# Kernel optimization log

Hardware: AMD Instinct MI355X
Metric: run time of the kernel (lower is better)

## Reference

```python
import jax, jax.numpy as jnp
import numpy as np

N, C, K, STEPS = 131072, 256, 5, 20


def setup_inputs() -> dict:
    key = jax.random.key(0)
    k1, k2, k3, k4 = jax.random.split(key, 4)
    drive = jax.random.uniform(k1, (N, C), dtype=jnp.float32)  # sigmoid-like drive in [0,1]
    K_raw = jax.random.uniform(k2, (K,), dtype=jnp.float32)
    K_local = K_raw / K_raw.sum()  # positive, sums to 1
    W = jax.random.uniform(k3, (C, C), dtype=jnp.float32)
    mask = (jax.random.uniform(k4, (C, C)) < 0.2).astype(jnp.float32)
    W = W * mask
    W_cc = W / jnp.clip(W.sum(axis=0, keepdims=True), 1e-8)  # column-stochastic
    r = jnp.full((C,), 3.9, dtype=jnp.float32)
    eps = jnp.full((C,), 0.3, dtype=jnp.float32)
    beta = jnp.full((C,), 0.1, dtype=jnp.float32)
    return {"drive": drive, "r": r, "eps": eps, "beta": beta,
            "K_local": K_local, "W_cc": W_cc}


def reference(drive, r, eps, beta, K_local, W_cc):
    # readout == 'final' (module default)
    pad = K // 2
    one_m_eps = 1.0 - eps
    one_m_beta = 1.0 - beta

    def step(grid, _):
        mapped = r * grid * (1.0 - grid)  # [N, C] logistic map
        # circular conv1d over channel axis (cross-correlation, kernel K_local)
        local = K_local[0] * jnp.roll(mapped, pad, axis=-1)
        for j in range(1, K):
            local = local + K_local[j] * jnp.roll(mapped, pad - j, axis=-1)
        global_cc = mapped @ W_cc  # [N, C]
        coupled = 0.5 * (local + global_cc)
        physics = one_m_eps * mapped + eps * coupled
        new_grid = one_m_beta * physics + beta * drive
        return new_grid, None

    grid, _ = jax.lax.scan(step, drive, None, length=STEPS)
    return jnp.clip(grid, 1e-4, 1.0 - 1e-4)
```

## Files before the change

kernel.cpp:

```cpp
#include <hip/hip_runtime.h>

#define C_DIM 256
#define STEPS 20
#define ROWS_PER_WG 32

typedef _Float16 f16;
typedef f16 f16x4 __attribute__((ext_vector_type(4)));
typedef f16 f16x8 __attribute__((ext_vector_type(8)));
typedef float f32x4 __attribute__((ext_vector_type(4)));

__global__ __launch_bounds__(256) void prep_w(const float* __restrict__ W,
                                              const float* __restrict__ Kl,
                                              f16* __restrict__ whi,
                                              f16* __restrict__ wlo)
{
    const int f = (int)(blockIdx.x * blockDim.x + threadIdx.x) >> 6;
    const int l = (int)threadIdx.x & 63;
    if (f >= 128) return;
    const int mt = f >> 3, kb = f & 7;
    const int n = mt * 16 + (l & 15);
    const int kbase = kb * 32 + (l >> 4) * 8;
    f16 h[8], lo[8];
    #pragma unroll
    for (int j = 0; j < 8; ++j) {
        const int k = kbase + j;
        float v = 0.5f * W[k * C_DIM + n];
        const int d = (k - n + 2) & (C_DIM - 1);
        if (d < 5) v += 0.5f * Kl[d];
        const f16 hh = (f16)v;
        h[j] = hh;
        lo[j] = (f16)((v - (float)hh) * 4096.0f);
    }
    const size_t off = (size_t)f * 512 + (size_t)l * 8;
    *(f16x8*)(whi + off) = *(f16x8*)h;
    *(f16x8*)(wlo + off) = *(f16x8*)lo;
}

__global__ __launch_bounds__(512, 2) void cml_main(
    const float* __restrict__ drive,
    const float* __restrict__ r_,
    const float* __restrict__ eps_,
    const float* __restrict__ beta_,
    const f16* __restrict__ whi,
    const f16* __restrict__ wlo,
    float* __restrict__ out)
{
    __shared__ char smem[65536];

    const int tid = (int)threadIdx.x;
    const int w   = tid >> 6;
    const int l   = tid & 63;
    const int kg  = l >> 4;
    const int cl  = l & 15;
    const size_t rowBase = (size_t)blockIdx.x * ROWS_PER_WG;

    f16x8 Wh[2][8], Wl[2][8];
    #pragma unroll
    for (int mti = 0; mti < 2; ++mti) {
        #pragma unroll
        for (int kb = 0; kb < 8; ++kb) {
            const size_t off = (size_t)((w * 2 + mti) * 8 + kb) * 512 + (size_t)l * 8;
            Wh[mti][kb] = *(const f16x8*)(whi + off);
            Wl[mti][kb] = *(const f16x8*)(wlo + off);
        }
    }

    float rr[2][4], P1[2][4], P2[2][4];
    #pragma unroll
    for (int mti = 0; mti < 2; ++mti) {
        const int ch0 = (w * 2 + mti) * 16 + kg * 4;
        #pragma unroll
        for (int r = 0; r < 4; ++r) {
            const int ch = ch0 + r;
            const float rv = r_[ch], ev = eps_[ch], bv = beta_[ch];
            rr[mti][r] = rv;
            P1[mti][r] = (1.0f - bv) * (1.0f - ev);
            P2[mti][r] = (1.0f - bv) * ev;
        }
    }

    float g[2][2][4], m_[2][2][4], drv[2][2][4];
    #pragma unroll
    for (int mti = 0; mti < 2; ++mti) {
        const int ch0 = (w * 2 + mti) * 16 + kg * 4;
        #pragma unroll
        for (int nt = 0; nt < 2; ++nt) {
            const size_t row = rowBase + (size_t)(nt * 16 + cl);
            const f32x4 d4 = *(const f32x4*)(drive + row * C_DIM + ch0);
            #pragma unroll
            for (int r = 0; r < 4; ++r) {
                const float bv = beta_[ch0 + r];
                g[mti][nt][r]   = d4[r];
                drv[mti][nt][r] = bv * d4[r];
            }
        }
    }

    int rbase[2], woff[2][2];
    #pragma unroll
    for (int nt = 0; nt < 2; ++nt) {
        const int m = nt * 16 + cl;
        rbase[nt] = (m << 9) + ((kg ^ (m & 7)) << 4);
        #pragma unroll
        for (int mti = 0; mti < 2; ++mti) {
            const int c = (w * 2 + mti) * 2 + (kg >> 1);
            const int p = c ^ (m & 7);
            woff[mti][nt] = (m << 9) + (p << 4) + ((kg & 1) << 3);
        }
    }

    #pragma unroll
    for (int mti = 0; mti < 2; ++mti) {
        #pragma unroll
        for (int nt = 0; nt < 2; ++nt) {
            f16x4 hv, lv;
            #pragma unroll
            for (int r = 0; r < 4; ++r) {
                const float gv = g[mti][nt][r];
                const float mv = rr[mti][r] * gv * (1.0f - gv);
                m_[mti][nt][r] = mv;
                const f16 hh = (f16)mv;
                hv[r] = hh;
                lv[r] = (f16)((mv - (float)hh) * 4096.0f);
            }
            *(f16x4*)(smem + woff[mti][nt]) = hv;
            *(f16x4*)(smem + woff[mti][nt] + 16384) = lv;
        }
    }

    #pragma unroll 1
    for (int s = 0; s < STEPS; ++s) {
        __syncthreads();
        const int rb = (s & 1) << 15;
        const int wb = rb ^ 32768;

        #pragma unroll
        for (int nt = 0; nt < 2; ++nt) {
            f32x4 acch[2], accl[2];
            #pragma unroll
            for (int mti = 0; mti < 2; ++mti) {
                acch[mti] = (f32x4)0.0f;
                accl[mti] = (f32x4)0.0f;
            }

            const int Ab = rbase[nt] | rb;
            #pragma unroll
            for (int kb = 0; kb < 8; ++kb) {
                const int addr = Ab ^ (kb << 6);
                const f16x8 bh = *(const f16x8*)(smem + addr);
                const f16x8 bl = *(const f16x8*)(smem + addr + 16384);
                #pragma unroll
                for (int mti = 0; mti < 2; ++mti) {
                    acch[mti] = __builtin_amdgcn_mfma_f32_16x16x32_f16(Wh[mti][kb], bh, acch[mti], 0, 0, 0);
                    accl[mti] = __builtin_amdgcn_mfma_f32_16x16x32_f16(Wl[mti][kb], bh, accl[mti], 0, 0, 0);
                    accl[mti] = __builtin_amdgcn_mfma_f32_16x16x32_f16(Wh[mti][kb], bl, accl[mti], 0, 0, 0);
                }
            }

            #pragma unroll
            for (int mti = 0; mti < 2; ++mti) {
                f16x4 hv, lv;
                #pragma unroll
                for (int r = 0; r < 4; ++r) {
                    const float coupled = fmaf(accl[mti][r], 1.0f / 4096.0f, acch[mti][r]);
                    const float gn = fmaf(P1[mti][r], m_[mti][nt][r],
                                     fmaf(P2[mti][r], coupled, drv[mti][nt][r]));
                    g[mti][nt][r] = gn;
                    const float mv = rr[mti][r] * gn * (1.0f - gn);
                    m_[mti][nt][r] = mv;
                    const f16 hh = (f16)mv;
                    hv[r] = hh;
                    lv[r] = (f16)((mv - (float)hh) * 4096.0f);
                }
                if (s != STEPS - 1) {
                    *(f16x4*)(smem + (woff[mti][nt] | wb)) = hv;
                    *(f16x4*)(smem + (woff[mti][nt] | wb) + 16384) = lv;
                }
            }
        }
    }

    #pragma unroll
    for (int mti = 0; mti < 2; ++mti) {
        const int ch0 = (w * 2 + mti) * 16 + kg * 4;
        #pragma unroll
        for (int nt = 0; nt < 2; ++nt) {
            const size_t row = rowBase + (size_t)(nt * 16 + cl);
            f32x4 o;
            #pragma unroll
            for (int r = 0; r < 4; ++r) {
                o[r] = fminf(fmaxf(g[mti][nt][r], 1e-4f), 1.0f - 1e-4f);
            }
            *(f32x4*)(out + row * C_DIM + ch0) = o;
        }
    }
}

extern "C" void kernel_launch(void* const* d_in, const int* in_sizes, int n_in,
                              void* d_out, int out_size, void* d_ws, size_t ws_size,
                              hipStream_t stream) {
    (void)n_in; (void)ws_size; (void)out_size;
    const float* drive = (const float*)d_in[0];
    const float* r     = (const float*)d_in[1];
    const float* eps   = (const float*)d_in[2];
    const float* beta  = (const float*)d_in[3];
    const float* Kl    = (const float*)d_in[4];
    const float* W     = (const float*)d_in[5];
    float* out = (float*)d_out;

    f16* whi = (f16*)d_ws;
    f16* wlo = whi + 65536;

    prep_w<<<dim3(32), dim3(256), 0, stream>>>(W, Kl, whi, wlo);

    const int nrows = in_sizes[0] / C_DIM;
    cml_main<<<dim3((unsigned)(nrows / ROWS_PER_WG)), dim3(512), 0, stream>>>(
        drive, r, eps, beta, whi, wlo, out);
}
```

Baseline: 721.1 us.

## Software-pipeline LDS B loads, stagger row tiles per wave, spill drive term to LDS

The inner MFMA loop now prefetches the next k-block's hi/lo B fragments from LDS while issuing the current MFMAs, and wraps the MFMA group in s_setprio. Half of the waves process the two row tiles in swapped order to spread LDS bank and port contention. The beta*drive term moves from registers into a per-thread LDS region to cut VGPR pressure, which needs dynamic shared memory of about 105 KB. That size may limit occupancy to one workgroup per CU where the launch bounds ask for two.

```diff
diff --git a/kernel.cpp b/kernel.cpp
--- a/kernel.cpp
+++ b/kernel.cpp
@@ -3,6 +3,8 @@
 #define C_DIM 256
 #define STEPS 20
 #define ROWS_PER_WG 32
+#define DRV_BASE 65536
+#define SMEM_BYTES (65536 + 512 * 80)
 
 typedef _Float16 f16;
 typedef f16 f16x4 __attribute__((ext_vector_type(4)));
@@ -45,14 +47,19 @@
     const f16* __restrict__ wlo,
     float* __restrict__ out)
 {
-    __shared__ char smem[65536];
+    extern __shared__ char smem[];
 
     const int tid = (int)threadIdx.x;
     const int w   = tid >> 6;
     const int l   = tid & 63;
     const int kg  = l >> 4;
     const int cl  = l & 15;
+    const int ntSwap = (w >> 2) & 1;
     const size_t rowBase = (size_t)blockIdx.x * ROWS_PER_WG;
+    const int drvBase = DRV_BASE + tid * 80;
+
+    const int ntm0 = ntSwap;
+    const int ntm1 = ntSwap ^ 1;
 
     f16x8 Wh[2][8], Wl[2][8];
     #pragma unroll
@@ -79,52 +86,56 @@
         }
     }
 
-    float g[2][2][4], m_[2][2][4], drv[2][2][4];
-    #pragma unroll
-    for (int mti = 0; mti < 2; ++mti) {
-        const int ch0 = (w * 2 + mti) * 16 + kg * 4;
-        #pragma unroll
-        for (int nt = 0; nt < 2; ++nt) {
-            const size_t row = rowBase + (size_t)(nt * 16 + cl);
-            const f32x4 d4 = *(const f32x4*)(drive + row * C_DIM + ch0);
-            #pragma unroll
-            for (int r = 0; r < 4; ++r) {
-                const float bv = beta_[ch0 + r];
-                g[mti][nt][r]   = d4[r];
-                drv[mti][nt][r] = bv * d4[r];
+    float g[2][2][4], m_[2][2][4];
+    {
+        const int mrow[2] = { ntm0 * 16 + cl, ntm1 * 16 + cl };
+        #pragma unroll
+        for (int mti = 0; mti < 2; ++mti) {
+            const int ch0 = (w * 2 + mti) * 16 + kg * 4;
+            #pragma unroll
+            for (int u = 0; u < 2; ++u) {
+                const size_t row = rowBase + (size_t)mrow[u];
+                const f32x4 d4 = *(const f32x4*)(drive + row * C_DIM + ch0);
+                f32x4 dv;
+                #pragma unroll
+                for (int r = 0; r < 4; ++r) {
+                    g[mti][u][r] = d4[r];
+                    dv[r] = beta_[ch0 + r] * d4[r];
+                }
+                *(f32x4*)(smem + drvBase + ((mti * 2 + u) << 4)) = dv;
             }
         }
     }
 
     int rbase[2], woff[2][2];
     #pragma unroll
-    for (int nt = 0; nt < 2; ++nt) {
-        const int m = nt * 16 + cl;
-        rbase[nt] = (m << 9) + ((kg ^ (m & 7)) << 4);
+    for (int u = 0; u < 2; ++u) {
+        const int m = (u ? ntm1 : ntm0) * 16 + cl;
+        rbase[u] = (m << 9) + ((kg ^ (m & 7)) << 4);
         #pragma unroll
         for (int mti = 0; mti < 2; ++mti) {
             const int c = (w * 2 + mti) * 2 + (kg >> 1);
             const int p = c ^ (m & 7);
-            woff[mti][nt] = (m << 9) + (p << 4) + ((kg & 1) << 3);
+            woff[mti][u] = (m << 9) + (p << 4) + ((kg & 1) << 3);
         }
     }
 
     #pragma unroll
     for (int mti = 0; mti < 2; ++mti) {
         #pragma unroll
-        for (int nt = 0; nt < 2; ++nt) {
+        for (int u = 0; u < 2; ++u) {
             f16x4 hv, lv;
             #pragma unroll
             for (int r = 0; r < 4; ++r) {
-                const float gv = g[mti][nt][r];
+                const float gv = g[mti][u][r];
                 const float mv = rr[mti][r] * gv * (1.0f - gv);
-                m_[mti][nt][r] = mv;
+                m_[mti][u][r] = mv;
                 const f16 hh = (f16)mv;
                 hv[r] = hh;
                 lv[r] = (f16)((mv - (float)hh) * 4096.0f);
             }
-            *(f16x4*)(smem + woff[mti][nt]) = hv;
-            *(f16x4*)(smem + woff[mti][nt] + 16384) = lv;
+            *(f16x4*)(smem + woff[mti][u]) = hv;
+            *(f16x4*)(smem + woff[mti][u] + 16384) = lv;
         }
     }
 
@@ -133,65 +144,80 @@
         __syncthreads();
         const int rb = (s & 1) << 15;
         const int wb = rb ^ 32768;
-
-        #pragma unroll
-        for (int nt = 0; nt < 2; ++nt) {
+        const int lastStep = (s == STEPS - 1);
+
+        const int Ab0 = rbase[0] | rb;
+        const int Ab1 = rbase[1] | rb;
+
+        f16x8 bh = *(const f16x8*)(smem + Ab0);
+        f16x8 bl = *(const f16x8*)(smem + Ab0 + 16384);
+
+        #pragma unroll
+        for (int u = 0; u < 2; ++u) {
+            const int Ab = u ? Ab1 : Ab0;
             f32x4 acch[2], accl[2];
+            acch[0] = (f32x4)0.0f; acch[1] = (f32x4)0.0f;
+            accl[0] = (f32x4)0.0f; accl[1] = (f32x4)0.0f;
+
+            #pragma unroll
+            for (int kb = 0; kb < 8; ++kb) {
+                f16x8 nbh, nbl;
+                const bool hasNext = (kb < 7) || (u == 0);
+                const int na = (kb < 7) ? (Ab ^ ((kb + 1) << 6)) : Ab1;
+                if (hasNext) {
+                    nbh = *(const f16x8*)(smem + na);
+                    nbl = *(const f16x8*)(smem + na + 16384);
+                }
+                __builtin_amdgcn_s_setprio(1);
+                acch[0] = __builtin_amdgcn_mfma_f32_16x16x32_f16(Wh[0][kb], bh, acch[0], 0, 0, 0);
+                acch[1] = __builtin_amdgcn_mfma_f32_16x16x32_f16(Wh[1][kb], bh, acch[1], 0, 0, 0);
+                accl[0] = __builtin_amdgcn_mfma_f32_16x16x32_f16(Wl[0][kb], bh, accl[0], 0, 0, 0);
+                accl[1] = __builtin_amdgcn_mfma_f32_16x16x32_f16(Wl[1][kb], bh, accl[1], 0, 0, 0);
+                accl[0] = __builtin_amdgcn_mfma_f32_16x16x32_f16(Wh[0][kb], bl, accl[0], 0, 0, 0);
+                accl[1] = __builtin_amdgcn_mfma_f32_16x16x32_f16(Wh[1][kb], bl, accl[1], 0, 0, 0);
+                __builtin_amdgcn_s_setprio(0);
+                if (hasNext) { bh = nbh; bl = nbl; }
+            }
+
             #pragma unroll
             for (int mti = 0; mti < 2; ++mti) {
-                acch[mti] = (f32x4)0.0f;
-                accl[mti] = (f32x4)0.0f;
-            }
-
-            const int Ab = rbase[nt] | rb;
-            #pragma unroll
-            for (int kb = 0; kb < 8; ++kb) {
-                const int addr = Ab ^ (kb << 6);
-                const f16x8 bh = *(const f16x8*)(smem + addr);
-                const f16x8 bl = *(const f16x8*)(smem + addr + 16384);
-                #pragma unroll
-                for (int mti = 0; mti < 2; ++mti) {
-                    acch[mti] = __builtin_amdgcn_mfma_f32_16x16x32_f16(Wh[mti][kb], bh, acch[mti], 0, 0, 0);
-                    accl[mti] = __builtin_amdgcn_mfma_f32_16x16x32_f16(Wl[mti][kb], bh, accl[mti], 0, 0, 0);
-                    accl[mti] = __builtin_amdgcn_mfma_f32_16x16x32_f16(Wh[mti][kb], bl, accl[mti], 0, 0, 0);
-                }
-            }
-
-            #pragma unroll
-            for (int mti = 0; mti < 2; ++mti) {
+                const f32x4 dv = *(const f32x4*)(smem + drvBase + ((mti * 2 + u) << 4));
                 f16x4 hv, lv;
                 #pragma unroll
                 for (int r = 0; r < 4; ++r) {
                     const float coupled = fmaf(accl[mti][r], 1.0f / 4096.0f, acch[mti][r]);
-                    const float gn = fmaf(P1[mti][r], m_[mti][nt][r],
-                                     fmaf(P2[mti][r], coupled, drv[mti][nt][r]));
-                    g[mti][nt][r] = gn;
+                    const float gn = fmaf(P1[mti][r], m_[mti][u][r],
+                                     fmaf(P2[mti][r], coupled, dv[r]));
+                    g[mti][u][r] = gn;
                     const float mv = rr[mti][r] * gn * (1.0f - gn);
-                    m_[mti][nt][r] = mv;
+                    m_[mti][u][r] = mv;
                     const f16 hh = (f16)mv;
                     hv[r] = hh;
                     lv[r] = (f16)((mv - (float)hh) * 4096.0f);
                 }
-                if (s != STEPS - 1) {
-                    *(f16x4*)(smem + (woff[mti][nt] | wb)) = hv;
-                    *(f16x4*)(smem + (woff[mti][nt] | wb) + 16384) = lv;
-                }
-            }
-        }
-    }
-
-    #pragma unroll
-    for (int mti = 0; mti < 2; ++mti) {
-        const int ch0 = (w * 2 + mti) * 16 + kg * 4;
-        #pragma unroll
-        for (int nt = 0; nt < 2; ++nt) {
-            const size_t row = rowBase + (size_t)(nt * 16 + cl);
-            f32x4 o;
-            #pragma unroll
-            for (int r = 0; r < 4; ++r) {
-                o[r] = fminf(fmaxf(g[mti][nt][r], 1e-4f), 1.0f - 1e-4f);
-            }
-            *(f32x4*)(out + row * C_DIM + ch0) = o;
+                if (!lastStep) {
+                    *(f16x4*)(smem + (woff[mti][u] | wb)) = hv;
+                    *(f16x4*)(smem + (woff[mti][u] | wb) + 16384) = lv;
+                }
+            }
+        }
+    }
+
+    {
+        const int mrow[2] = { ntm0 * 16 + cl, ntm1 * 16 + cl };
+        #pragma unroll
+        for (int mti = 0; mti < 2; ++mti) {
+            const int ch0 = (w * 2 + mti) * 16 + kg * 4;
+            #pragma unroll
+            for (int u = 0; u < 2; ++u) {
+                const size_t row = rowBase + (size_t)mrow[u];
+                f32x4 o;
+                #pragma unroll
+                for (int r = 0; r < 4; ++r) {
+                    o[r] = fminf(fmaxf(g[mti][u][r], 1e-4f), 1.0f - 1e-4f);
+                }
+                *(f32x4*)(out + row * C_DIM + ch0) = o;
+            }
         }
     }
 }
@@ -213,7 +239,10 @@
 
     prep_w<<<dim3(32), dim3(256), 0, stream>>>(W, Kl, whi, wlo);
 
+    hipFuncSetAttribute((const void*)cml_main,
+                        hipFuncAttributeMaxDynamicSharedMemorySize, SMEM_BYTES);
+
     const int nrows = in_sizes[0] / C_DIM;
-    cml_main<<<dim3((unsigned)(nrows / ROWS_PER_WG)), dim3(512), 0, stream>>>(
+    cml_main<<<dim3((unsigned)(nrows / ROWS_PER_WG)), dim3(512), SMEM_BYTES, stream>>>(
         drive, r, eps, beta, whi, wlo, out);
 }
```

New measurement: 721.9 us. No clear change (+0.1%).
